# Optimization experiments

Hardware: AMD Instinct MI355X
Metric: run time of the kernel (lower is better)

The kernel has to match this reference:

```python
import jax, jax.numpy as jnp
import numpy as np

B, T, D_IN, H, LAT = 256, 512, 32, 128, 64


def lstm_scan(x, Wih, Whh, bih, bhh):
    """PyTorch-convention single-layer LSTM over x [B,T,D] -> hidden states [B,T,H].
    Gate order: i, f, g, o. Gates = x@Wih.T + bih + h@Whh.T + bhh."""
    Bm, _, _ = x.shape
    Hm = Whh.shape[1]
    # precompute input contributions for all timesteps: [B,T,4H]
    xg = jnp.einsum('btd,gd->btg', x, Wih) + bih + bhh

    def step(carry, g_t):
        h, c = carry
        gates = g_t + h @ Whh.T  # [B,4H]
        i, f, g, o = jnp.split(gates, 4, axis=-1)
        i = jax.nn.sigmoid(i)
        f = jax.nn.sigmoid(f)
        g = jnp.tanh(g)
        o = jax.nn.sigmoid(o)
        c = f * c + i * g
        h = o * jnp.tanh(c)
        return (h, c), h

    h0 = jnp.zeros((Bm, Hm), x.dtype)
    (_, _), hs = jax.lax.scan(step, (h0, h0), jnp.swapaxes(xg, 0, 1))
    return jnp.swapaxes(hs, 0, 1)  # [B,T,H]


def setup_inputs() -> dict:
    key = jax.random.key(0)
    ks = jax.random.split(key, 14)
    s = 1.0 / np.sqrt(H)

    def u(k, shape):
        return jax.random.uniform(k, shape, jnp.float32, -s, s)

    return {
        'x': jax.random.normal(ks[0], (B, T, D_IN), jnp.float32),
        # encoder LSTM (input_dim -> hidden)
        'enc_Wih': u(ks[1], (4 * H, D_IN)),
        'enc_Whh': u(ks[2], (4 * H, H)),
        'enc_bih': u(ks[3], (4 * H,)),
        'enc_bhh': u(ks[4], (4 * H,)),
        # encoder linear (hidden -> latent)
        'enc_Wl': u(ks[5], (LAT, H)),
        'enc_bl': u(ks[6], (LAT,)),
        # decoder LSTM (latent -> hidden)
        'dec_Wih': u(ks[7], (4 * H, LAT)),
        'dec_Whh': u(ks[8], (4 * H, H)),
        'dec_bih': u(ks[9], (4 * H,)),
        'dec_bhh': u(ks[10], (4 * H,)),
        # decoder linear (hidden -> input_dim)
        'dec_Wl': u(ks[11], (D_IN, H)),
        'dec_bl': u(ks[12], (D_IN,)),
    }


def reference(x, enc_Wih, enc_Whh, enc_bih, enc_bhh, enc_Wl, enc_bl,
              dec_Wih, dec_Whh, dec_bih, dec_bhh, dec_Wl, dec_bl):
    # Encoder: last hidden state -> linear -> latent
    hs = lstm_scan(x, enc_Wih, enc_Whh, enc_bih, enc_bhh)  # [B,T,H]
    h_last = hs[:, -1]                                     # == hidden.squeeze(0)
    encoded = h_last @ enc_Wl.T + enc_bl                   # [B,LAT]
    # Decoder: repeat latent over time, LSTM, linear
    z = jnp.broadcast_to(encoded[:, None, :], (encoded.shape[0], T, encoded.shape[1]))
    hs2 = lstm_scan(z, dec_Wih, dec_Whh, dec_bih, dec_bhh)  # [B,T,H]
    decoded = hs2 @ dec_Wl.T + dec_bl                       # [B,T,D_IN]
    return encoded, decoded
```

## Files before the change

### kernel.cpp

```cpp
#include <hip/hip_runtime.h>

#define NB   256
#define NT   512
#define NDIN 32
#define NH   128
#define NLAT 64
#define HSTR 132

typedef _Float16 h2 __attribute__((ext_vector_type(2)));
typedef _Float16 h4 __attribute__((ext_vector_type(4)));

__device__ __forceinline__ float dot2(h2 a, h2 b, float c) {
  return __builtin_amdgcn_fdot2(a, b, c, false);
}
__device__ __forceinline__ h2 bc2(float v) { return __builtin_bit_cast(h2, v); }
__device__ __forceinline__ h2 pk2(float a, float b) { return h2{(_Float16)a, (_Float16)b}; }

__device__ __forceinline__ float fast_rcp(float x) { return __builtin_amdgcn_rcpf(x); }
__device__ __forceinline__ float sigmoid_f(float x) { return fast_rcp(1.f + __expf(-x)); }
__device__ __forceinline__ float tanh_f(float x) {
  float ax = fabsf(x);
  float e  = __expf(-2.f * ax);
  float t  = (1.f - e) * fast_rcp(1.f + e);
  return copysignf(t, x);
}

template <int CTRL>
__device__ __forceinline__ float dpp_add(float v) {
  int s = __builtin_bit_cast(int, v);
  int p = __builtin_amdgcn_update_dpp(0, s, CTRL, 0xF, 0xF, true);
  return v + __builtin_bit_cast(float, p);
}
__device__ __forceinline__ float quad_reduce(float v) {
  v = dpp_add<0xB1>(v);
  v = dpp_add<0x4E>(v);
  return v;
}

__global__ __launch_bounds__(512, 2) void lstm_ae_kernel(
    const float* __restrict__ x,
    const float* __restrict__ eWih,
    const float* __restrict__ eWhh,
    const float* __restrict__ eBih,
    const float* __restrict__ eBhh,
    const float* __restrict__ eWl,
    const float* __restrict__ eBl,
    const float* __restrict__ dWih,
    const float* __restrict__ dWhh,
    const float* __restrict__ dBih,
    const float* __restrict__ dBhh,
    const float* __restrict__ dWl,
    const float* __restrict__ dBl,
    float* __restrict__ outE,
    float* __restrict__ outD)
{
  extern __shared__ __align__(16) char smem[];
  float*    h32s = (float*)smem;
  float*    encs = h32s + NH;
  _Float16* hbuf = (_Float16*)(encs + NLAT);
  _Float16* hist = hbuf + 2 * NH;
  _Float16* xs   = hist;

  const int tid = threadIdx.x;
  const int b   = blockIdx.x;
  const int Q   = tid & 3;
  const int J   = tid >> 2;

  {
    const float4* xg = (const float4*)(x + (size_t)b * (NT * NDIN));
    h4* xo = (h4*)xs;
#pragma unroll
    for (int i = 0; i < 8; ++i) {
      int idx = i * 512 + tid;
      float4 v = xg[idx];
      xo[idx] = h4{(_Float16)v.x, (_Float16)v.y, (_Float16)v.z, (_Float16)v.w};
    }
  }

  h2 wh[4][16];
  h2 wi[4][4];
  float bias[4];
#pragma unroll
  for (int G = 0; G < 4; ++G) {
    const float4* p = (const float4*)(eWhh + (size_t)(G * NH + J) * NH + Q * 32);
#pragma unroll
    for (int f = 0; f < 8; ++f) {
      float4 v = p[f];
      wh[G][2 * f] = pk2(v.x, v.y); wh[G][2 * f + 1] = pk2(v.z, v.w);
    }
    const float4* q = (const float4*)(eWih + (size_t)(G * NH + J) * NDIN + Q * 8);
#pragma unroll
    for (int f = 0; f < 2; ++f) {
      float4 v = q[f];
      wi[G][2 * f] = pk2(v.x, v.y); wi[G][2 * f + 1] = pk2(v.z, v.w);
    }
    bias[G] = eBih[G * NH + J] + eBhh[G * NH + J];
  }
  if (tid < NH) hbuf[tid] = (_Float16)0.f;
  float c = 0.f;
  __syncthreads();

#pragma unroll 1
  for (int t = 0; t < NT; ++t) {
    float a0 = 0.f, a1 = 0.f, a2 = 0.f, a3 = 0.f;
    const float4* hp = (const float4*)(hbuf + (t & 1) * NH + Q * 32);
#pragma unroll
    for (int r = 0; r < 4; ++r) {
      float4 hv = hp[r];
      h2 p0 = bc2(hv.x), p1 = bc2(hv.y), p2 = bc2(hv.z), p3 = bc2(hv.w);
      a0 = dot2(wh[0][4*r+0], p0, a0); a0 = dot2(wh[0][4*r+1], p1, a0);
      a0 = dot2(wh[0][4*r+2], p2, a0); a0 = dot2(wh[0][4*r+3], p3, a0);
      a1 = dot2(wh[1][4*r+0], p0, a1); a1 = dot2(wh[1][4*r+1], p1, a1);
      a1 = dot2(wh[1][4*r+2], p2, a1); a1 = dot2(wh[1][4*r+3], p3, a1);
      a2 = dot2(wh[2][4*r+0], p0, a2); a2 = dot2(wh[2][4*r+1], p1, a2);
      a2 = dot2(wh[2][4*r+2], p2, a2); a2 = dot2(wh[2][4*r+3], p3, a2);
      a3 = dot2(wh[3][4*r+0], p0, a3); a3 = dot2(wh[3][4*r+1], p1, a3);
      a3 = dot2(wh[3][4*r+2], p2, a3); a3 = dot2(wh[3][4*r+3], p3, a3);
    }
    {
      float4 xv = *(const float4*)(xs + t * NDIN + Q * 8);
      h2 p0 = bc2(xv.x), p1 = bc2(xv.y), p2 = bc2(xv.z), p3 = bc2(xv.w);
      a0 = dot2(wi[0][0], p0, a0); a0 = dot2(wi[0][1], p1, a0);
      a0 = dot2(wi[0][2], p2, a0); a0 = dot2(wi[0][3], p3, a0);
      a1 = dot2(wi[1][0], p0, a1); a1 = dot2(wi[1][1], p1, a1);
      a1 = dot2(wi[1][2], p2, a1); a1 = dot2(wi[1][3], p3, a1);
      a2 = dot2(wi[2][0], p0, a2); a2 = dot2(wi[2][1], p1, a2);
      a2 = dot2(wi[2][2], p2, a2); a2 = dot2(wi[2][3], p3, a2);
      a3 = dot2(wi[3][0], p0, a3); a3 = dot2(wi[3][1], p1, a3);
      a3 = dot2(wi[3][2], p2, a3); a3 = dot2(wi[3][3], p3, a3);
    }
    a0 = quad_reduce(a0) + bias[0];
    a1 = quad_reduce(a1) + bias[1];
    a2 = quad_reduce(a2) + bias[2];
    a3 = quad_reduce(a3) + bias[3];
    float gi = sigmoid_f(a0), gf = sigmoid_f(a1);
    float gg = tanh_f(a2),    go = sigmoid_f(a3);
    c = fmaf(gf, c, gi * gg);
    float h = go * tanh_f(c);
    if (Q == 0) {
      hbuf[((t + 1) & 1) * NH + J] = (_Float16)h;
      if (t == NT - 1) h32s[J] = h;
    }
    __syncthreads();
  }

  if (tid < NLAT) {
    const float4* p  = (const float4*)(eWl + (size_t)tid * NH);
    const float4* hh = (const float4*)h32s;
    float a = eBl[tid];
#pragma unroll
    for (int r = 0; r < 32; ++r) {
      float4 w = p[r]; float4 hv = hh[r];
      a = fmaf(hv.x, w.x, a); a = fmaf(hv.y, w.y, a);
      a = fmaf(hv.z, w.z, a); a = fmaf(hv.w, w.w, a);
    }
    encs[tid] = a;
    outE[b * NLAT + tid] = a;
  }
#pragma unroll
  for (int G = 0; G < 4; ++G) {
    const float4* p = (const float4*)(dWhh + (size_t)(G * NH + J) * NH + Q * 32);
#pragma unroll
    for (int f = 0; f < 8; ++f) {
      float4 v = p[f];
      wh[G][2 * f] = pk2(v.x, v.y); wh[G][2 * f + 1] = pk2(v.z, v.w);
    }
  }
  if (tid < NH) hbuf[tid] = (_Float16)0.f;
  c = 0.f;
  __syncthreads();

  float xgd[4];
  {
    const float4* ep = (const float4*)(encs + Q * 16);
    float4 e0 = ep[0], e1 = ep[1], e2 = ep[2], e3 = ep[3];
#pragma unroll
    for (int G = 0; G < 4; ++G) {
      const float4* p = (const float4*)(dWih + (size_t)(G * NH + J) * NLAT + Q * 16);
      float4 w0 = p[0], w1 = p[1], w2 = p[2], w3 = p[3];
      float a;
      a = e0.x * w0.x;        a = fmaf(e0.y, w0.y, a);
      a = fmaf(e0.z, w0.z, a); a = fmaf(e0.w, w0.w, a);
      a = fmaf(e1.x, w1.x, a); a = fmaf(e1.y, w1.y, a);
      a = fmaf(e1.z, w1.z, a); a = fmaf(e1.w, w1.w, a);
      a = fmaf(e2.x, w2.x, a); a = fmaf(e2.y, w2.y, a);
      a = fmaf(e2.z, w2.z, a); a = fmaf(e2.w, w2.w, a);
      a = fmaf(e3.x, w3.x, a); a = fmaf(e3.y, w3.y, a);
      a = fmaf(e3.z, w3.z, a); a = fmaf(e3.w, w3.w, a);
      xgd[G] = quad_reduce(a) + dBih[G * NH + J] + dBhh[G * NH + J];
    }
  }

#pragma unroll 1
  for (int t = 0; t < NT; ++t) {
    float a0 = 0.f, a1 = 0.f, a2 = 0.f, a3 = 0.f;
    const float4* hp = (const float4*)(hbuf + (t & 1) * NH + Q * 32);
#pragma unroll
    for (int r = 0; r < 4; ++r) {
      float4 hv = hp[r];
      h2 p0 = bc2(hv.x), p1 = bc2(hv.y), p2 = bc2(hv.z), p3 = bc2(hv.w);
      a0 = dot2(wh[0][4*r+0], p0, a0); a0 = dot2(wh[0][4*r+1], p1, a0);
      a0 = dot2(wh[0][4*r+2], p2, a0); a0 = dot2(wh[0][4*r+3], p3, a0);
      a1 = dot2(wh[1][4*r+0], p0, a1); a1 = dot2(wh[1][4*r+1], p1, a1);
      a1 = dot2(wh[1][4*r+2], p2, a1); a1 = dot2(wh[1][4*r+3], p3, a1);
      a2 = dot2(wh[2][4*r+0], p0, a2); a2 = dot2(wh[2][4*r+1], p1, a2);
      a2 = dot2(wh[2][4*r+2], p2, a2); a2 = dot2(wh[2][4*r+3], p3, a2);
      a3 = dot2(wh[3][4*r+0], p0, a3); a3 = dot2(wh[3][4*r+1], p1, a3);
      a3 = dot2(wh[3][4*r+2], p2, a3); a3 = dot2(wh[3][4*r+3], p3, a3);
    }
    a0 = quad_reduce(a0) + xgd[0];
    a1 = quad_reduce(a1) + xgd[1];
    a2 = quad_reduce(a2) + xgd[2];
    a3 = quad_reduce(a3) + xgd[3];
    float gi = sigmoid_f(a0), gf = sigmoid_f(a1);
    float gg = tanh_f(a2),    go = sigmoid_f(a3);
    c = fmaf(gf, c, gi * gg);
    float h = go * tanh_f(c);
    if (Q == 0) {
      _Float16 hh = (_Float16)h;
      hbuf[((t + 1) & 1) * NH + J] = hh;
      hist[t * HSTR + J] = hh;
    }
    __syncthreads();
  }

  {
    const int cg = tid >> 5, rl = tid & 31, c0 = 2 * cg;
    h2 wl0[64], wl1[64];
    const float4* p0 = (const float4*)(dWl + (size_t)c0 * NH);
    const float4* p1 = (const float4*)(dWl + (size_t)(c0 + 1) * NH);
#pragma unroll
    for (int f = 0; f < 32; ++f) {
      float4 v0 = p0[f]; wl0[2*f] = pk2(v0.x, v0.y); wl0[2*f+1] = pk2(v0.z, v0.w);
      float4 v1 = p1[f]; wl1[2*f] = pk2(v1.x, v1.y); wl1[2*f+1] = pk2(v1.z, v1.w);
    }
    const float bo0 = dBl[c0], bo1 = dBl[c0 + 1];
    float* op = outD + (size_t)b * (NT * NDIN);
#pragma unroll 1
    for (int i = 0; i < 16; ++i) {
      int r = rl + 32 * i;
      const float2* hp = (const float2*)(hist + r * HSTR);
      float s0 = 0.f, s1 = 0.f;
#pragma unroll
      for (int j = 0; j < 32; ++j) {
        float2 hv = hp[j];
        h2 lo = bc2(hv.x), hi = bc2(hv.y);
        s0 = dot2(wl0[2*j], lo, s0); s0 = dot2(wl0[2*j+1], hi, s0);
        s1 = dot2(wl1[2*j], lo, s1); s1 = dot2(wl1[2*j+1], hi, s1);
      }
      *(float2*)(op + (size_t)r * NDIN + c0) = make_float2(s0 + bo0, s1 + bo1);
    }
  }
}

#define SMEM_BYTES ((NH + NLAT) * 4 + 2 * NH * 2 + NT * HSTR * 2)

extern "C" void kernel_launch(void* const* d_in, const int* in_sizes, int n_in,
                              void* d_out, int out_size, void* d_ws, size_t ws_size,
                              hipStream_t stream) {
  const float* x    = (const float*)d_in[0];
  const float* eWih = (const float*)d_in[1];
  const float* eWhh = (const float*)d_in[2];
  const float* eBih = (const float*)d_in[3];
  const float* eBhh = (const float*)d_in[4];
  const float* eWl  = (const float*)d_in[5];
  const float* eBl  = (const float*)d_in[6];
  const float* dWih = (const float*)d_in[7];
  const float* dWhh = (const float*)d_in[8];
  const float* dBih = (const float*)d_in[9];
  const float* dBhh = (const float*)d_in[10];
  const float* dWl  = (const float*)d_in[11];
  const float* dBl  = (const float*)d_in[12];

  float* outE = (float*)d_out;
  float* outD = outE + (size_t)NB * NLAT;

  (void)hipFuncSetAttribute((const void*)lstm_ae_kernel,
                            hipFuncAttributeMaxDynamicSharedMemorySize,
                            SMEM_BYTES);

  hipLaunchKernelGGL(lstm_ae_kernel, dim3(NB), dim3(512), SMEM_BYTES, stream,
                     x, eWih, eWhh, eBih, eBhh, eWl, eBl,
                     dWih, dWhh, dBih, dBhh, dWl, dBl, outE, outD);
}
```

Measured before the change: 704.5 us.

## Simplify activations, drop fp32 final-hidden buffer, remap output projection threads

Rewrites sigmoid and tanh to use exp2 plus reciprocal, with tanh expressed as 2*sigmoid(2x)-1 so the abs and copysign steps disappear. The encoder's final hidden state is now read from the fp16 ping-pong buffer instead of a separate fp32 copy, which removes a per-step branch but lowers the precision of the latent input. The decoder output projection maps each thread to one output column over strided rows, reading history with 16-byte loads, and the history row stride is widened to 136 halves, presumably for alignment and bank behaviour. Synchronisation around the decoder setup is rearranged.

Measured after the change: 679.3 us. 1.04x faster.

```diff
diff --git a/kernel.cpp b/kernel.cpp
--- a/kernel.cpp
+++ b/kernel.cpp
@@ -5,7 +5,7 @@
 #define NDIN 32
 #define NH   128
 #define NLAT 64
-#define HSTR 132
+#define HSTR 136
 
 typedef _Float16 h2 __attribute__((ext_vector_type(2)));
 typedef _Float16 h4 __attribute__((ext_vector_type(4)));
@@ -16,13 +16,13 @@
 __device__ __forceinline__ h2 bc2(float v) { return __builtin_bit_cast(h2, v); }
 __device__ __forceinline__ h2 pk2(float a, float b) { return h2{(_Float16)a, (_Float16)b}; }
 
-__device__ __forceinline__ float fast_rcp(float x) { return __builtin_amdgcn_rcpf(x); }
-__device__ __forceinline__ float sigmoid_f(float x) { return fast_rcp(1.f + __expf(-x)); }
+#define NLOG2E 1.44269504f
+__device__ __forceinline__ float sigmoid_f(float x) {
+  return __builtin_amdgcn_rcpf(1.f + __builtin_amdgcn_exp2f(x * -NLOG2E));
+}
 __device__ __forceinline__ float tanh_f(float x) {
-  float ax = fabsf(x);
-  float e  = __expf(-2.f * ax);
-  float t  = (1.f - e) * fast_rcp(1.f + e);
-  return copysignf(t, x);
+  float s = __builtin_amdgcn_rcpf(1.f + __builtin_amdgcn_exp2f(x * (-2.f * NLOG2E)));
+  return fmaf(2.f, s, -1.f);
 }
 
 template <int CTRL>
@@ -55,8 +55,7 @@
     float* __restrict__ outD)
 {
   extern __shared__ __align__(16) char smem[];
-  float*    h32s = (float*)smem;
-  float*    encs = h32s + NH;
+  float*    encs = (float*)smem;
   _Float16* hbuf = (_Float16*)(encs + NLAT);
   _Float16* hist = hbuf + 2 * NH;
   _Float16* xs   = hist;
@@ -137,22 +136,21 @@
     float gg = tanh_f(a2),    go = sigmoid_f(a3);
     c = fmaf(gf, c, gi * gg);
     float h = go * tanh_f(c);
-    if (Q == 0) {
-      hbuf[((t + 1) & 1) * NH + J] = (_Float16)h;
-      if (t == NT - 1) h32s[J] = h;
-    }
+    if (Q == 0) hbuf[((t + 1) & 1) * NH + J] = (_Float16)h;
     __syncthreads();
   }
 
   if (tid < NLAT) {
     const float4* p  = (const float4*)(eWl + (size_t)tid * NH);
-    const float4* hh = (const float4*)h32s;
+    const float2* hh = (const float2*)hbuf;
     float a = eBl[tid];
 #pragma unroll
     for (int r = 0; r < 32; ++r) {
-      float4 w = p[r]; float4 hv = hh[r];
-      a = fmaf(hv.x, w.x, a); a = fmaf(hv.y, w.y, a);
-      a = fmaf(hv.z, w.z, a); a = fmaf(hv.w, w.w, a);
+      float4 w = p[r];
+      float2 hv = hh[r];
+      h2 lo = bc2(hv.x), hi = bc2(hv.y);
+      a = fmaf((float)lo.x, w.x, a); a = fmaf((float)lo.y, w.y, a);
+      a = fmaf((float)hi.x, w.z, a); a = fmaf((float)hi.y, w.w, a);
     }
     encs[tid] = a;
     outE[b * NLAT + tid] = a;
@@ -166,10 +164,10 @@
       wh[G][2 * f] = pk2(v.x, v.y); wh[G][2 * f + 1] = pk2(v.z, v.w);
     }
   }
+  __syncthreads();
+
   if (tid < NH) hbuf[tid] = (_Float16)0.f;
   c = 0.f;
-  __syncthreads();
-
   float xgd[4];
   {
     const float4* ep = (const float4*)(encs + Q * 16);
@@ -190,6 +188,7 @@
       xgd[G] = quad_reduce(a) + dBih[G * NH + J] + dBhh[G * NH + J];
     }
   }
+  __syncthreads();
 
 #pragma unroll 1
   for (int t = 0; t < NT; ++t) {
@@ -225,35 +224,35 @@
   }
 
   {
-    const int cg = tid >> 5, rl = tid & 31, c0 = 2 * cg;
-    h2 wl0[64], wl1[64];
-    const float4* p0 = (const float4*)(dWl + (size_t)c0 * NH);
-    const float4* p1 = (const float4*)(dWl + (size_t)(c0 + 1) * NH);
+    const int col = tid & 31, rg = tid >> 5;
+    h2 wl[64];
+    const float4* p0 = (const float4*)(dWl + (size_t)col * NH);
 #pragma unroll
     for (int f = 0; f < 32; ++f) {
-      float4 v0 = p0[f]; wl0[2*f] = pk2(v0.x, v0.y); wl0[2*f+1] = pk2(v0.z, v0.w);
-      float4 v1 = p1[f]; wl1[2*f] = pk2(v1.x, v1.y); wl1[2*f+1] = pk2(v1.z, v1.w);
-    }
-    const float bo0 = dBl[c0], bo1 = dBl[c0 + 1];
+      float4 v = p0[f];
+      wl[2 * f] = pk2(v.x, v.y); wl[2 * f + 1] = pk2(v.z, v.w);
+    }
+    const float bo = dBl[col];
     float* op = outD + (size_t)b * (NT * NDIN);
 #pragma unroll 1
-    for (int i = 0; i < 16; ++i) {
-      int r = rl + 32 * i;
-      const float2* hp = (const float2*)(hist + r * HSTR);
-      float s0 = 0.f, s1 = 0.f;
-#pragma unroll
-      for (int j = 0; j < 32; ++j) {
-        float2 hv = hp[j];
-        h2 lo = bc2(hv.x), hi = bc2(hv.y);
-        s0 = dot2(wl0[2*j], lo, s0); s0 = dot2(wl0[2*j+1], hi, s0);
-        s1 = dot2(wl1[2*j], lo, s1); s1 = dot2(wl1[2*j+1], hi, s1);
+    for (int i = 0; i < 32; ++i) {
+      int r = rg + 16 * i;
+      const float4* hp = (const float4*)(hist + r * HSTR);
+      float s = 0.f;
+#pragma unroll
+      for (int j = 0; j < 16; ++j) {
+        float4 hv = hp[j];
+        s = dot2(wl[4*j+0], bc2(hv.x), s);
+        s = dot2(wl[4*j+1], bc2(hv.y), s);
+        s = dot2(wl[4*j+2], bc2(hv.z), s);
+        s = dot2(wl[4*j+3], bc2(hv.w), s);
       }
-      *(float2*)(op + (size_t)r * NDIN + c0) = make_float2(s0 + bo0, s1 + bo1);
-    }
-  }
-}
-
-#define SMEM_BYTES ((NH + NLAT) * 4 + 2 * NH * 2 + NT * HSTR * 2)
+      op[(size_t)r * NDIN + col] = s + bo;
+    }
+  }
+}
+
+#define SMEM_BYTES (NLAT * 4 + 2 * NH * 2 + NT * HSTR * 2)
 
 extern "C" void kernel_launch(void* const* d_in, const int* in_sizes, int n_in,
                               void* d_out, int out_size, void* d_ws, size_t ws_size,
```
